# Performance work log

Hardware: AMD Instinct MI355X
Metric: run time of the kernel (lower is better)

## Reference

```python
import jax, jax.numpy as jnp
import numpy as np

B, S, D = 4, 2048, 1024
N_HEAD = 16
D_HEAD = D // N_HEAD
WINDOW = 1024
D_FF = 4 * D
EPS = 1e-5
NEG = -1e10


def _layernorm(x, g, b):
    mu = jnp.mean(x, axis=-1, keepdims=True)
    var = jnp.mean(jnp.square(x - mu), axis=-1, keepdims=True)
    return (x - mu) * jax.lax.rsqrt(var + EPS) * g + b


def setup_inputs() -> dict:
    key = jax.random.key(0)
    ks = jax.random.split(key, 12)
    s = 1.0 / np.sqrt(D)
    x = jax.random.normal(ks[0], (B, S, D), dtype=jnp.float32)
    key_pad_mask = jax.random.bernoulli(ks[1], 0.1, (B, S))
    return {
        "x": x,
        "key_pad_mask": key_pad_mask,
        "ln1_g": jnp.ones((D,), jnp.float32),
        "ln1_b": jnp.zeros((D,), jnp.float32),
        "wq": jax.random.normal(ks[2], (D, D), jnp.float32) * s,
        "bq": jnp.zeros((D,), jnp.float32),
        "wkv": jax.random.normal(ks[3], (D, 2 * D), jnp.float32) * s,
        "bkv": jnp.zeros((2 * D,), jnp.float32),
        "ln2_g": jnp.ones((D,), jnp.float32),
        "ln2_b": jnp.zeros((D,), jnp.float32),
        "w1": jax.random.normal(ks[4], (D, D_FF), jnp.float32) * s,
        "b1": jnp.zeros((D_FF,), jnp.float32),
        "w2": jax.random.normal(ks[5], (D_FF, D), jnp.float32) * (1.0 / np.sqrt(D_FF)),
        "b2": jnp.zeros((D,), jnp.float32),
    }


def reference(x, key_pad_mask, ln1_g, ln1_b, wq, bq, wkv, bkv, ln2_g, ln2_b, w1, b1, w2, b2):
    ln1x = _layernorm(x, ln1_g, ln1_b)
    # queries over full sequence: [B, S, nh, dh]
    q = (ln1x @ wq + bq).reshape(B, S, N_HEAD, D_HEAD)
    # keys/values from the last WINDOW tokens: [B, W, 2*nh, dh]
    kv = (ln1x[:, -WINDOW:, :] @ wkv + bkv).reshape(B, WINDOW, 2 * N_HEAD, D_HEAD)
    k, v = kv[..., :N_HEAD, :], kv[..., N_HEAD:, :]
    # NOTE: original scales by sqrt(embed_dim), not sqrt(head_dim)
    scores = jnp.einsum('bqhd,bkhd->bhqk', q, k) / np.sqrt(D)
    causal = jnp.triu(jnp.ones((S, WINDOW), dtype=bool), k=1)  # faithful to original
    pad = key_pad_mask[:, None, None, -WINDOW:]
    scores = jnp.where(pad | causal[None, None], jnp.float32(NEG), scores)
    attn = jax.nn.softmax(scores, axis=-1)
    out = jnp.einsum('bhqk,bkhd->bqhd', attn, v).reshape(B, S, D)
    h = _layernorm(out, ln2_g, ln2_b)
    h = jax.nn.silu(h @ w1 + b1) @ w2 + b2
    return h + x
```

## Files before the change

### kernel.cpp

```cpp
#include <hip/hip_runtime.h>
#include <hip/hip_bf16.h>

#define BB 4
#define SS 2048
#define DD 1024
#define HH 16
#define DHH 64
#define WW 1024
#define DFF 4096
#define MM (BB*SS)
#define NEGV (-1e10f)
#define KSC 0.045084220027780106f

using f32x4 = __attribute__((ext_vector_type(4))) float;
using s16x8 = __attribute__((ext_vector_type(8))) short;
using s16x4 = __attribute__((ext_vector_type(4))) short;
using u64 = unsigned long long;

typedef const __attribute__((address_space(1))) void* gas_t;
typedef __attribute__((address_space(3))) void* las_t;

__device__ inline short f2b(float f) {
  __hip_bfloat16 h = __float2bfloat16(f);
  return __builtin_bit_cast(short, h);
}
__device__ inline float b2f(short u) {
  __hip_bfloat16 h = __builtin_bit_cast(__hip_bfloat16, u);
  return __bfloat162float(h);
}

__device__ inline void gload_lds16(const short* g, short* lds) {
  __builtin_amdgcn_global_load_lds((gas_t)g, (las_t)lds, 16, 0, 0);
}

__device__ inline f32x4 mfma16(s16x8 a, s16x8 b, f32x4 c) {
  return __builtin_amdgcn_mfma_f32_16x16x32_bf16(a, b, c, 0, 0, 0);
}

template<int IN_BF16>
__global__ __launch_bounds__(256) void ln_kernel(const void* __restrict__ inp,
                                                 const float* __restrict__ g,
                                                 const float* __restrict__ bta,
                                                 short* __restrict__ outp) {
  int row = blockIdx.x;
  int t = threadIdx.x;
  float v[4];
  if constexpr (IN_BF16) {
    s16x4 r4 = *((const s16x4*)((const short*)inp + (size_t)row*DD) + t);
    v[0]=b2f(r4[0]); v[1]=b2f(r4[1]); v[2]=b2f(r4[2]); v[3]=b2f(r4[3]);
  } else {
    f32x4 r4 = *((const f32x4*)((const float*)inp + (size_t)row*DD) + t);
    v[0]=r4[0]; v[1]=r4[1]; v[2]=r4[2]; v[3]=r4[3];
  }
  float s = v[0]+v[1]+v[2]+v[3];
  float sq = v[0]*v[0]+v[1]*v[1]+v[2]*v[2]+v[3]*v[3];
  for (int m=1;m<64;m<<=1){ s += __shfl_xor(s,m); sq += __shfl_xor(sq,m); }
  __shared__ float red[8];
  int wv = t>>6;
  if ((t&63)==0){ red[wv]=s; red[4+wv]=sq; }
  __syncthreads();
  s  = red[0]+red[1]+red[2]+red[3];
  sq = red[4]+red[5]+red[6]+red[7];
  float mean = s*(1.f/DD);
  float rstd = rsqrtf(sq*(1.f/DD) - mean*mean + 1e-5f);
  int col = t*4;
  s16x4 o;
  #pragma unroll
  for (int j=0;j<4;++j) o[j] = f2b((v[j]-mean)*rstd*g[col+j]+bta[col+j]);
  *((s16x4*)(outp + (size_t)row*DD) + t) = o;
}

__global__ __launch_bounds__(256) void transpose_cast(const float* __restrict__ in,
                                                      short* __restrict__ out,
                                                      int K, int N) {
  __shared__ float tile[32][33];
  int n0 = blockIdx.x*32, k0 = blockIdx.y*32;
  int tx = threadIdx.x & 31, ty = threadIdx.x >> 5;
  #pragma unroll
  for (int j=0;j<4;++j) tile[ty+8*j][tx] = in[(size_t)(k0+ty+8*j)*N + n0+tx];
  __syncthreads();
  #pragma unroll
  for (int j=0;j<4;++j) out[(size_t)(n0+ty+8*j)*K + k0+tx] = f2b(tile[tx][ty+8*j]);
}

__global__ void pad_bitmask(const int* __restrict__ pad, u64* __restrict__ pm) {
  int idx = threadIdx.x;
  int b_ = idx>>4, col = idx&15;
  const int* pb = pad + b_*SS + (SS-WW);
  u64 m = 0;
  for (int c=0;c<16;++c)
    for (int nf=0;nf<4;++nf)
      if (pb[c*64+nf*16+col]) m |= (1ull << (c*4+nf));
  pm[idx] = m;
}

template<int EPI>
__global__ __launch_bounds__(512) void gemm256(const short* __restrict__ A,
                                               const short* __restrict__ Bt,
                                               const float* __restrict__ bias,
                                               void* __restrict__ out1,
                                               int N, int K, int lgx) {
  __shared__ short lds[49152];
  int tid = threadIdx.x, l = tid&63, wid = tid>>6;
  int wm = wid>>2, wn = wid&3;
  int q8 = gridDim.x >> 3;
  int wg = (blockIdx.x & 7)*q8 + (blockIdx.x >> 3);
  int bx = wg & ((1<<lgx)-1), by = wg >> lgx;
  const short* Ablk = A + (size_t)by*256*K;
  const short* Bblk = Bt + (size_t)bx*256*K;
  int rA = l & 15;
  int slot_s = ((l>>4) ^ ((rA>>1)&3))*8;
  int aBase = (wm*128 + rA)*32 + slot_s;
  int bBase = (wn*64  + rA)*32 + slot_s + 8192;
  int qs = (tid&3) ^ ((tid>>3)&3);
  const short* srcA = Ablk + (size_t)(tid>>2)*K + qs*8;
  const short* srcB = Bblk + (size_t)(tid>>2)*K + qs*8;
  int dst0 = (tid & ~63)*8;
  int nt = K >> 5;
  f32x4 acc[8][4];
  #pragma unroll
  for (int i=0;i<8;++i)
    #pragma unroll
    for (int j=0;j<4;++j)
      #pragma unroll
      for (int r=0;r<4;++r) acc[i][j][r]=0.f;

  auto stage = [&](int isB, int rgn, int t) {
    const short* s = isB ? srcB : srcA;
    short* d = &lds[rgn*16384 + isB*8192 + dst0];
    gload_lds16(s + t*32,                 d);
    gload_lds16(s + (size_t)128*K + t*32, d + 4096);
  };
  s16x8 af[4], bf[4];
  auto readA = [&](int rgn, int mg) {
    #pragma unroll
    for (int j=0;j<4;++j) af[j] = *(const s16x8*)&lds[rgn*16384 + aBase + (mg*4+j)*512];
  };
  auto readB = [&](int rgn) {
    #pragma unroll
    for (int j=0;j<4;++j) bf[j] = *(const s16x8*)&lds[rgn*16384 + bBase + j*512];
  };
  auto mfmas = [&](int mg) {
    __builtin_amdgcn_s_setprio(1);
    #pragma unroll
    for (int j=0;j<4;++j)
      #pragma unroll
      for (int nf=0;nf<4;++nf)
        acc[mg*4+j][nf] = mfma16(af[j], bf[nf], acc[mg*4+j][nf]);
    __builtin_amdgcn_s_setprio(0);
  };

  stage(0,0,0); stage(1,0,0);
  stage(0,1,1); stage(1,1,1);
  asm volatile("s_waitcnt vmcnt(4)" ::: "memory");
  __builtin_amdgcn_s_barrier();

  int cur = 0, s2 = 2;
  for (int t = 0; t < nt; ++t) {
    int ts = t+2; if (ts >= nt) ts -= nt;
    readB(cur); readA(cur,0);
    stage(0, s2, ts);
    __builtin_amdgcn_s_barrier();
    mfmas(0);
    __builtin_amdgcn_s_barrier();
    readA(cur,1);
    stage(1, s2, ts);
    __builtin_amdgcn_s_barrier();
    mfmas(1);
    asm volatile("s_waitcnt vmcnt(4)" ::: "memory");
    __builtin_amdgcn_s_barrier();
    cur = (cur+1==3) ? 0 : cur+1;
    s2  = (s2+1==3)  ? 0 : s2+1;
  }
  asm volatile("s_waitcnt vmcnt(0)" ::: "memory");

  #pragma unroll
  for (int mf=0;mf<8;++mf) {
    #pragma unroll
    for (int nf=0;nf<4;++nf) {
      #pragma unroll
      for (int r=0;r<4;++r) {
        int row = by*256 + wm*128 + mf*16 + ((l>>4)<<2) + r;
        int col = bx*256 + wn*64 + nf*16 + rA;
        float v = acc[mf][nf][r] + bias[col];
        if constexpr (EPI==2) {
          float sv = v / (1.f + __expf(-v));
          ((short*)out1)[(size_t)row*N + col] = f2b(sv);
        } else {
          ((short*)out1)[(size_t)row*N + col] = f2b(v);
        }
      }
    }
  }
}

template<int EPI>
__global__ __launch_bounds__(512) void gemm256x128(const short* __restrict__ A,
                                                   const short* __restrict__ Bt,
                                                   const float* __restrict__ bias,
                                                   void* __restrict__ out1,
                                                   void* __restrict__ out2,
                                                   const float* __restrict__ resid,
                                                   int N, int K, int lgx) {
  __shared__ short lds[24576];
  int tid = threadIdx.x, l = tid&63, wid = tid>>6;
  int wm = wid>>1, wn = wid&1;
  int q8 = gridDim.x >> 3;
  int wg = (blockIdx.x & 7)*q8 + (blockIdx.x >> 3);
  int bx = wg & ((1<<lgx)-1), by = wg >> lgx;
  const short* Ablk;
  if constexpr (EPI==1) {
    int b_ = (by*256)>>10, w0 = (by*256)&1023;
    Ablk = A + ((size_t)b_*SS + (SS-WW) + w0)*DD;
  } else {
    Ablk = A + (size_t)by*256*K;
  }
  const short* Bblk = Bt + (size_t)bx*128*K;
  int rA = l & 15;
  int slot_s = ((l>>4) ^ ((rA>>1)&3))*8;
  int aBase = (wm*64 + rA)*32 + slot_s;
  int bBase = 8192 + (wn*64 + rA)*32 + slot_s;
  int qs = (tid&3) ^ ((tid>>3)&3);
  const short* srcA = Ablk + (size_t)(tid>>2)*K + qs*8;
  const short* srcB = Bblk + (size_t)(tid>>2)*K + qs*8;
  int dst0 = (tid & ~63)*8;
  int nt = K >> 5;
  f32x4 acc[4][4];
  #pragma unroll
  for (int i=0;i<4;++i)
    #pragma unroll
    for (int j=0;j<4;++j)
      #pragma unroll
      for (int r=0;r<4;++r) acc[i][j][r]=0.f;

  auto stageA = [&](int b, int t) {
    short* d = &lds[b*12288 + dst0];
    gload_lds16(srcA + t*32,                 d);
    gload_lds16(srcA + (size_t)128*K + t*32, d + 4096);
  };
  auto stageB = [&](int b, int t) {
    gload_lds16(srcB + t*32, &lds[b*12288 + 8192 + dst0]);
  };
  s16x8 af[2], bf[4];
  auto readA = [&](int b, int mg) {
    #pragma unroll
    for (int j=0;j<2;++j) af[j] = *(const s16x8*)&lds[b*12288 + aBase + (mg*2+j)*512];
  };
  auto readB = [&](int b) {
    #pragma unroll
    for (int j=0;j<4;++j) bf[j] = *(const s16x8*)&lds[b*12288 + bBase + j*512];
  };
  auto mfmas = [&](int mg) {
    __builtin_amdgcn_s_setprio(1);
    #pragma unroll
    for (int j=0;j<2;++j)
      #pragma unroll
      for (int nf=0;nf<4;++nf)
        acc[mg*2+j][nf] = mfma16(af[j], bf[nf], acc[mg*2+j][nf]);
    __builtin_amdgcn_s_setprio(0);
  };

  stageA(0,0); stageB(0,0); stageB(1,1);
  asm volatile("s_waitcnt vmcnt(1)" ::: "memory");
  __builtin_amdgcn_s_barrier();

  for (int it = 0; it < (nt>>1); ++it) {
    int t0 = 2*it;
    int t2 = t0+2; if (t2 >= nt) t2 -= nt;
    int t3 = t0+3; if (t3 >= nt) t3 -= nt;
    readB(0); readA(0,0);
    stageA(1,t0+1);
    __builtin_amdgcn_s_barrier();
    mfmas(0);
    __builtin_amdgcn_s_barrier();
    readA(0,1);
    stageB(0,t2);
    __builtin_amdgcn_s_barrier();
    mfmas(1);
    asm volatile("s_waitcnt vmcnt(1)" ::: "memory");
    __builtin_amdgcn_s_barrier();
    readB(1); readA(1,0);
    stageA(0,t2);
    __builtin_amdgcn_s_barrier();
    mfmas(0);
    __builtin_amdgcn_s_barrier();
    readA(1,1);
    stageB(1,t3);
    __builtin_amdgcn_s_barrier();
    mfmas(1);
    asm volatile("s_waitcnt vmcnt(1)" ::: "memory");
    __builtin_amdgcn_s_barrier();
  }
  asm volatile("s_waitcnt vmcnt(0)" ::: "memory");

  #pragma unroll
  for (int mf=0;mf<4;++mf) {
    #pragma unroll
    for (int nf=0;nf<4;++nf) {
      #pragma unroll
      for (int r=0;r<4;++r) {
        int row = by*256 + wm*64 + mf*16 + ((l>>4)<<2) + r;
        int col = bx*128 + wn*64 + nf*16 + rA;
        float v = acc[mf][nf][r] + bias[col];
        if constexpr (EPI==0) {
          ((short*)out1)[(size_t)row*N + col] = f2b(v);
        } else if constexpr (EPI==1) {
          int b_ = row>>10, w_ = row&1023;
          if (col < DD) {
            int h = col>>6, dh = col&63;
            ((short*)out1)[(((size_t)(b_*HH+h))*WW + w_)*DHH + dh] = f2b(v*KSC);
          } else {
            int cc = col - DD;
            int h = cc>>6, dh = cc&63;
            ((short*)out2)[(((size_t)(b_*HH+h))*DHH + dh)*WW + w_] = f2b(v);
          }
        } else {
          ((float*)out1)[(size_t)row*N + col] = v + resid[(size_t)row*N + col];
        }
      }
    }
  }
}

struct KF { s16x8 v[4][2]; };

__global__ __launch_bounds__(64,2) void attn_kernel(const short* __restrict__ q,
    const short* __restrict__ kpan, const short* __restrict__ vtpan,
    const u64* __restrict__ pmarr, short* __restrict__ outp) {
  __shared__ short P[32*72];
  int l = threadIdx.x;
  int id = blockIdx.x;
  int xcd = id & 7, slot = id >> 3;
  int bh = xcd + 8*(slot >> 6);
  int u  = 63 - (slot & 63);
  int bb = bh >> 4, h = bh & 15;
  int r0 = u*32;
  const short* kbase = kpan + (size_t)bh*WW*DHH;
  const short* vbase = vtpan + (size_t)bh*DHH*WW;
  u64 pmask = pmarr[bb*16 + (l&15)];
  const s16x8 ones8 = { 0x3F80,0x3F80,0x3F80,0x3F80,0x3F80,0x3F80,0x3F80,0x3F80 };

  s16x8 aq[2][2];
  #pragma unroll
  for (int g=0;g<2;++g)
    #pragma unroll
    for (int kf=0;kf<2;++kf)
      aq[g][kf] = *(const s16x8*)(q + ((size_t)bb*SS + r0 + g*16 + (l&15))*DD
                                    + h*DHH + (l>>4)*8 + kf*32);
  f32x4 oacc[2][4];
  float mrun[2][4], lrun[2][4], scale[2][4];
  #pragma unroll
  for (int g=0;g<2;++g)
    #pragma unroll
    for (int i=0;i<4;++i) {
      #pragma unroll
      for (int r=0;r<4;++r) oacc[g][i][r]=0.f;
      mrun[g][i]=-INFINITY; lrun[g][i]=0.f;
    }
  int dchunk = u>>1;
  int nch = dchunk+1 < 16 ? dchunk+1 : 16;

  auto loadK = [&](int c, KF& d) {
    const short* kc = kbase + (size_t)c*64*DHH;
    #pragma unroll
    for (int nf=0;nf<4;++nf) {
      const short* p = kc + (size_t)(nf*16+(l&15))*DHH + ((l>>4)*8);
      d.v[nf][0] = *(const s16x8*)p;
      d.v[nf][1] = *(const s16x8*)(p+32);
    }
  };

  auto body = [&](int c, KF& kf) {
    f32x4 sc[2][4];
    #pragma unroll
    for (int g=0;g<2;++g)
      #pragma unroll
      for (int nf=0;nf<4;++nf)
        #pragma unroll
        for (int r=0;r<4;++r) sc[g][nf][r]=0.f;
    __builtin_amdgcn_s_setprio(1);
    #pragma unroll
    for (int nf=0;nf<4;++nf)
      #pragma unroll
      for (int g=0;g<2;++g) {
        sc[g][nf] = mfma16(aq[g][0], kf.v[nf][0], sc[g][nf]);
        sc[g][nf] = mfma16(aq[g][1], kf.v[nf][1], sc[g][nf]);
      }
    __builtin_amdgcn_s_setprio(0);
    unsigned nib = (unsigned)(pmask >> (c*4)) & 15u;
    float pm[2][4];
    #pragma unroll
    for (int g=0;g<2;++g)
      #pragma unroll
      for (int r=0;r<4;++r) pm[g][r] = -INFINITY;
    if (c >= dchunk) {
      #pragma unroll
      for (int nf=0;nf<4;++nf) {
        int j = c*64 + nf*16 + (l&15);
        int padj = (int)((nib>>nf)&1u);
        #pragma unroll
        for (int g=0;g<2;++g)
          #pragma unroll
          for (int r=0;r<4;++r) {
            int sq_ = r0 + g*16 + ((l>>4)<<2) + r;
            float xv = (padj || (j > sq_)) ? NEGV : sc[g][nf][r];
            sc[g][nf][r] = xv;
            pm[g][r] = fmaxf(pm[g][r], xv);
          }
      }
    } else {
      #pragma unroll
      for (int nf=0;nf<4;++nf) {
        int padj = (int)((nib>>nf)&1u);
        #pragma unroll
        for (int g=0;g<2;++g)
          #pragma unroll
          for (int r=0;r<4;++r) {
            float xv = padj ? NEGV : sc[g][nf][r];
            sc[g][nf][r] = xv;
            pm[g][r] = fmaxf(pm[g][r], xv);
          }
      }
    }
    s16x8 vf0[4], vf1[4];
    #pragma unroll
    for (int nf=0;nf<4;++nf)
      vf0[nf] = *(const s16x8*)(vbase + (size_t)(nf*16+(l&15))*WW
                                + c*64 + ((l>>4)*8));
    int need = 0;
    #pragma unroll
    for (int g=0;g<2;++g)
      #pragma unroll
      for (int r=0;r<4;++r) need |= (pm[g][r] > mrun[g][r] + 12.f) ? 1 : 0;
    #pragma unroll
    for (int g=0;g<2;++g)
      #pragma unroll
      for (int r=0;r<4;++r) scale[g][r] = 1.f;
    if (__any(need)) {
      #pragma unroll
      for (int m=1;m<16;m<<=1)
        #pragma unroll
        for (int g=0;g<2;++g)
          #pragma unroll
          for (int r=0;r<4;++r) pm[g][r] = fmaxf(pm[g][r], __shfl_xor(pm[g][r], m));
      #pragma unroll
      for (int g=0;g<2;++g)
        #pragma unroll
        for (int r=0;r<4;++r) {
          float mn = fmaxf(mrun[g][r], pm[g][r]);
          scale[g][r] = exp2f(mrun[g][r]-mn);
          mrun[g][r] = mn;
        }
      #pragma unroll
      for (int g=0;g<2;++g)
        #pragma unroll
        for (int nf=0;nf<4;++nf)
          #pragma unroll
          for (int r=0;r<4;++r) oacc[g][nf][r] *= scale[g][r];
    }
    #pragma unroll
    for (int nf=0;nf<4;++nf)
      #pragma unroll
      for (int g=0;g<2;++g)
        #pragma unroll
        for (int r=0;r<4;++r)
          sc[g][nf][r] = exp2f(sc[g][nf][r]-mrun[g][r]);
    #pragma unroll
    for (int nf=0;nf<4;++nf)
      vf1[nf] = *(const s16x8*)(vbase + (size_t)(nf*16+(l&15))*WW
                                + c*64 + 32 + ((l>>4)*8));
    #pragma unroll
    for (int g=0;g<2;++g)
      #pragma unroll
      for (int nf=0;nf<4;++nf)
        #pragma unroll
        for (int r=0;r<4;++r)
          P[(g*16+((l>>4)<<2)+r)*72 + nf*16 + (l&15)] = f2b(sc[g][nf][r]);
    f32x4 ls2[2];
    #pragma unroll
    for (int g=0;g<2;++g)
      #pragma unroll
      for (int r=0;r<4;++r) ls2[g][r]=0.f;
    __builtin_amdgcn_s_setprio(1);
    #pragma unroll
    for (int ks=0;ks<2;++ks) {
      s16x8 ap[2];
      #pragma unroll
      for (int g=0;g<2;++g) {
        ap[g] = *(const s16x8*)&P[(g*16+(l&15))*72 + ks*32 + ((l>>4)*8)];
        ls2[g] = mfma16(ap[g], ones8, ls2[g]);
      }
      #pragma unroll
      for (int nf=0;nf<4;++nf) {
        s16x8 bv = ks ? vf1[nf] : vf0[nf];
        #pragma unroll
        for (int g=0;g<2;++g)
          oacc[g][nf] = mfma16(ap[g], bv, oacc[g][nf]);
      }
    }
    __builtin_amdgcn_s_setprio(0);
    #pragma unroll
    for (int g=0;g<2;++g)
      #pragma unroll
      for (int r=0;r<4;++r) lrun[g][r] = lrun[g][r]*scale[g][r] + ls2[g][r];
  };

  KF ka, kb;
  loadK(0, ka);
  int cend = nch, c = 0, ext = 0;
  while (true) {
    if (c == cend) {
      if (ext) break;
      ext = 1;
      int dead = 0;
      #pragma unroll
      for (int g=0;g<2;++g)
        #pragma unroll
        for (int r=0;r<4;++r) dead |= (mrun[g][r] < -5e9f) ? 1 : 0;
      if (!__any(dead)) break;
      cend = 16;
      if (c >= 16) break;
    }
    if (c+1 < 16) loadK(c+1, kb);
    body(c, ka);
    ka = kb;
    ++c;
  }

  #pragma unroll
  for (int g=0;g<2;++g)
    #pragma unroll
    for (int nf=0;nf<4;++nf)
      #pragma unroll
      for (int r=0;r<4;++r) {
        int srow = r0 + g*16 + ((l>>4)<<2) + r;
        float o = oacc[g][nf][r] / lrun[g][r];
        outp[((size_t)bb*SS + srow)*DD + h*DHH + nf*16 + (l&15)] = f2b(o);
      }
}

extern "C" void kernel_launch(void* const* d_in, const int* in_sizes, int n_in,
                              void* d_out, int out_size, void* d_ws, size_t ws_size,
                              hipStream_t stream) {
  const float* x    = (const float*)d_in[0];
  const int*   pad  = (const int*)d_in[1];
  const float* ln1g = (const float*)d_in[2];
  const float* ln1b = (const float*)d_in[3];
  const float* wq   = (const float*)d_in[4];
  const float* bq   = (const float*)d_in[5];
  const float* wkv  = (const float*)d_in[6];
  const float* bkv  = (const float*)d_in[7];
  const float* ln2g = (const float*)d_in[8];
  const float* ln2b = (const float*)d_in[9];
  const float* w1   = (const float*)d_in[10];
  const float* b1   = (const float*)d_in[11];
  const float* w2   = (const float*)d_in[12];
  const float* b2   = (const float*)d_in[13];

  char* ws = (char*)d_ws;
  const size_t MB = 1024*1024;
  short* ln1x = (short*)(ws + 0);
  short* qb   = (short*)(ws + 16*MB);
  short* kpan = (short*)(ws + 32*MB);
  short* vtp  = (short*)(ws + 40*MB);
  u64*   pmar = (u64*)  (ws + 48*MB);
  short* h1   = (short*)(ws + 0);
  short* outb = (short*)(ws + 64*MB);
  short* hb   = (short*)(ws + 80*MB);
  short* wqT  = (short*)(ws + 96*MB);
  short* wkvT = (short*)(ws + 98*MB);
  short* w1T  = (short*)(ws + 102*MB);
  short* w2T  = (short*)(ws + 110*MB);

  pad_bitmask<<<1,64,0,stream>>>(pad, pmar);
  transpose_cast<<<dim3(32,32),  256,0,stream>>>(wq,  wqT,  1024, 1024);
  transpose_cast<<<dim3(64,32),  256,0,stream>>>(wkv, wkvT, 1024, 2048);
  transpose_cast<<<dim3(128,32), 256,0,stream>>>(w1,  w1T,  1024, 4096);
  transpose_cast<<<dim3(32,128), 256,0,stream>>>(w2,  w2T,  4096, 1024);
  ln_kernel<0><<<MM,256,0,stream>>>(x, ln1g, ln1b, ln1x);
  gemm256x128<0><<<256,512,0,stream>>>(ln1x, wqT,  bq,  qb,   nullptr, nullptr, 1024, 1024, 3);
  gemm256x128<1><<<256,512,0,stream>>>(ln1x, wkvT, bkv, kpan, vtp,     nullptr, 2048, 1024, 4);
  attn_kernel<<<4096,64,0,stream>>>(qb, kpan, vtp, pmar, outb);
  ln_kernel<1><<<MM,256,0,stream>>>(outb, ln2g, ln2b, hb);
  gemm256<2><<<512,512,0,stream>>>(hb, w1T, b1, h1, 4096, 1024, 4);
  gemm256x128<3><<<256,512,0,stream>>>(h1, w2T, b2, d_out, nullptr, x, 1024, 4096, 3);
}
```

Before: 372.2 us.

## Simplify GEMM main loops to single-barrier triple-buffered pipeline

Both GEMM kernels drop their ping-pong/interleaved half-step scheduling, which used four barriers per K tile. Each now reads the whole A and B fragment set from LDS once, issues the next-next tile's global-to-LDS loads, runs all MFMAs and synchronizes with one barrier. The 256x128 kernel moves from a double-buffered scheme with split A/B staging to a three-region ring, so its LDS allocation grows. The aim is fewer barriers per K step, at the cost of more registers for fragments and less interleaving of LDS reads with MFMAs.

```diff
diff --git a/kernel.cpp b/kernel.cpp
--- a/kernel.cpp
+++ b/kernel.cpp
@@ -125,52 +125,39 @@
       #pragma unroll
       for (int r=0;r<4;++r) acc[i][j][r]=0.f;
 
-  auto stage = [&](int isB, int rgn, int t) {
-    const short* s = isB ? srcB : srcA;
-    short* d = &lds[rgn*16384 + isB*8192 + dst0];
-    gload_lds16(s + t*32,                 d);
-    gload_lds16(s + (size_t)128*K + t*32, d + 4096);
+  auto stage = [&](int rgn, int t) {
+    short* dA = &lds[rgn*16384 + dst0];
+    gload_lds16(srcA + t*32,                 dA);
+    gload_lds16(srcA + (size_t)128*K + t*32, dA + 4096);
+    short* dB = &lds[rgn*16384 + 8192 + dst0];
+    gload_lds16(srcB + t*32,                 dB);
+    gload_lds16(srcB + (size_t)128*K + t*32, dB + 4096);
   };
-  s16x8 af[4], bf[4];
-  auto readA = [&](int rgn, int mg) {
-    #pragma unroll
-    for (int j=0;j<4;++j) af[j] = *(const s16x8*)&lds[rgn*16384 + aBase + (mg*4+j)*512];
-  };
-  auto readB = [&](int rgn) {
-    #pragma unroll
-    for (int j=0;j<4;++j) bf[j] = *(const s16x8*)&lds[rgn*16384 + bBase + j*512];
-  };
-  auto mfmas = [&](int mg) {
-    __builtin_amdgcn_s_setprio(1);
-    #pragma unroll
-    for (int j=0;j<4;++j)
-      #pragma unroll
-      for (int nf=0;nf<4;++nf)
-        acc[mg*4+j][nf] = mfma16(af[j], bf[nf], acc[mg*4+j][nf]);
-    __builtin_amdgcn_s_setprio(0);
-  };
-
-  stage(0,0,0); stage(1,0,0);
-  stage(0,1,1); stage(1,1,1);
+
+  stage(0,0); stage(1,1);
   asm volatile("s_waitcnt vmcnt(4)" ::: "memory");
   __builtin_amdgcn_s_barrier();
 
-  int cur = 0, s2 = 2;
+  int cur = 0, nx = 2;
   for (int t = 0; t < nt; ++t) {
     int ts = t+2; if (ts >= nt) ts -= nt;
-    readB(cur); readA(cur,0);
-    stage(0, s2, ts);
-    __builtin_amdgcn_s_barrier();
-    mfmas(0);
-    __builtin_amdgcn_s_barrier();
-    readA(cur,1);
-    stage(1, s2, ts);
-    __builtin_amdgcn_s_barrier();
-    mfmas(1);
+    s16x8 af[8], bf[4];
+    #pragma unroll
+    for (int j=0;j<4;++j) bf[j] = *(const s16x8*)&lds[cur*16384 + bBase + j*512];
+    #pragma unroll
+    for (int j=0;j<8;++j) af[j] = *(const s16x8*)&lds[cur*16384 + aBase + j*512];
+    stage(nx, ts);
+    __builtin_amdgcn_s_setprio(1);
+    #pragma unroll
+    for (int j=0;j<8;++j)
+      #pragma unroll
+      for (int nf=0;nf<4;++nf)
+        acc[j][nf] = mfma16(af[j], bf[nf], acc[j][nf]);
+    __builtin_amdgcn_s_setprio(0);
     asm volatile("s_waitcnt vmcnt(4)" ::: "memory");
     __builtin_amdgcn_s_barrier();
     cur = (cur+1==3) ? 0 : cur+1;
-    s2  = (s2+1==3)  ? 0 : s2+1;
+    nx  = (nx+1==3)  ? 0 : nx+1;
   }
   asm volatile("s_waitcnt vmcnt(0)" ::: "memory");
 
@@ -202,7 +189,7 @@
                                                    void* __restrict__ out2,
                                                    const float* __restrict__ resid,
                                                    int N, int K, int lgx) {
-  __shared__ short lds[24576];
+  __shared__ short lds[36864];
   int tid = threadIdx.x, l = tid&63, wid = tid>>6;
   int wm = wid>>1, wn = wid&1;
   int q8 = gridDim.x >> 3;
@@ -233,63 +220,37 @@
       #pragma unroll
       for (int r=0;r<4;++r) acc[i][j][r]=0.f;
 
-  auto stageA = [&](int b, int t) {
-    short* d = &lds[b*12288 + dst0];
-    gload_lds16(srcA + t*32,                 d);
-    gload_lds16(srcA + (size_t)128*K + t*32, d + 4096);
+  auto stage = [&](int rgn, int t) {
+    short* dA = &lds[rgn*12288 + dst0];
+    gload_lds16(srcA + t*32,                 dA);
+    gload_lds16(srcA + (size_t)128*K + t*32, dA + 4096);
+    gload_lds16(srcB + t*32, &lds[rgn*12288 + 8192 + dst0]);
   };
-  auto stageB = [&](int b, int t) {
-    gload_lds16(srcB + t*32, &lds[b*12288 + 8192 + dst0]);
-  };
-  s16x8 af[2], bf[4];
-  auto readA = [&](int b, int mg) {
-    #pragma unroll
-    for (int j=0;j<2;++j) af[j] = *(const s16x8*)&lds[b*12288 + aBase + (mg*2+j)*512];
-  };
-  auto readB = [&](int b) {
-    #pragma unroll
-    for (int j=0;j<4;++j) bf[j] = *(const s16x8*)&lds[b*12288 + bBase + j*512];
-  };
-  auto mfmas = [&](int mg) {
+
+  stage(0,0); stage(1,1);
+  asm volatile("s_waitcnt vmcnt(3)" ::: "memory");
+  __builtin_amdgcn_s_barrier();
+
+  int cur = 0, nx = 2;
+  for (int t = 0; t < nt; ++t) {
+    int ts = t+2; if (ts >= nt) ts -= nt;
+    s16x8 af[4], bf[4];
+    #pragma unroll
+    for (int j=0;j<4;++j) bf[j] = *(const s16x8*)&lds[cur*12288 + bBase + j*512];
+    #pragma unroll
+    for (int j=0;j<4;++j) af[j] = *(const s16x8*)&lds[cur*12288 + aBase + j*512];
+    stage(nx, ts);
     __builtin_amdgcn_s_setprio(1);
     #pragma unroll
-    for (int j=0;j<2;++j)
+    for (int j=0;j<4;++j)
       #pragma unroll
       for (int nf=0;nf<4;++nf)
-        acc[mg*2+j][nf] = mfma16(af[j], bf[nf], acc[mg*2+j][nf]);
+        acc[j][nf] = mfma16(af[j], bf[nf], acc[j][nf]);
     __builtin_amdgcn_s_setprio(0);
-  };
-
-  stageA(0,0); stageB(0,0); stageB(1,1);
-  asm volatile("s_waitcnt vmcnt(1)" ::: "memory");
-  __builtin_amdgcn_s_barrier();
-
-  for (int it = 0; it < (nt>>1); ++it) {
-    int t0 = 2*it;
-    int t2 = t0+2; if (t2 >= nt) t2 -= nt;
-    int t3 = t0+3; if (t3 >= nt) t3 -= nt;
-    readB(0); readA(0,0);
-    stageA(1,t0+1);
+    asm volatile("s_waitcnt vmcnt(3)" ::: "memory");
     __builtin_amdgcn_s_barrier();
-    mfmas(0);
-    __builtin_amdgcn_s_barrier();
-    readA(0,1);
-    stageB(0,t2);
-    __builtin_amdgcn_s_barrier();
-    mfmas(1);
-    asm volatile("s_waitcnt vmcnt(1)" ::: "memory");
-    __builtin_amdgcn_s_barrier();
-    readB(1); readA(1,0);
-    stageA(0,t2);
-    __builtin_amdgcn_s_barrier();
-    mfmas(0);
-    __builtin_amdgcn_s_barrier();
-    readA(1,1);
-    stageB(1,t3);
-    __builtin_amdgcn_s_barrier();
-    mfmas(1);
-    asm volatile("s_waitcnt vmcnt(1)" ::: "memory");
-    __builtin_amdgcn_s_barrier();
+    cur = (cur+1==3) ? 0 : cur+1;
+    nx  = (nx+1==3)  ? 0 : nx+1;
   }
   asm volatile("s_waitcnt vmcnt(0)" ::: "memory");
 
```

New measurement: 374.7 us. About the same (+0.7%).
